# Optimization experiments

Hardware: AMD Instinct MI355X
Metric: run time of the kernel (lower is better)

The kernel has to match this reference:

```python
import jax, jax.numpy as jnp
import numpy as np

N, T, IN = 20000, 30, 32
H = 64          # lstm hidden
HEADS = 4
OUT = 32
E = 320000
NEG_SLOPE = 0.2


def _lstm_layer(x, Wih, Whh, bih, bhh):
    # x: [N, T, in]; Wih: [in, 4H]; Whh: [H, 4H]
    n, t, _ = x.shape
    h_dim = Whh.shape[0]
    xW = x @ Wih + bih  # [N, T, 4H]
    xW = jnp.transpose(xW, (1, 0, 2))  # [T, N, 4H]

    def step(carry, xt):
        h, c = carry
        g = xt + h @ Whh + bhh
        i, f, gg, o = jnp.split(g, 4, axis=-1)  # torch gate order i,f,g,o
        i = jax.nn.sigmoid(i)
        f = jax.nn.sigmoid(f)
        gg = jnp.tanh(gg)
        o = jax.nn.sigmoid(o)
        c = f * c + i * gg
        h = o * jnp.tanh(c)
        return (h, c), h

    init = (jnp.zeros((n, h_dim), x.dtype), jnp.zeros((n, h_dim), x.dtype))
    _, hs = jax.lax.scan(step, init, xW)
    return jnp.transpose(hs, (1, 0, 2))  # [N, T, H]


def _gat(x, edge_index, W, att_src, att_dst, bias, n):
    # x: [N, F_in]; W: [F_in, heads*C]; att_*: [heads, C]
    heads, C = att_src.shape
    h = (x @ W).reshape(n, heads, C)
    src, dst = edge_index[0], edge_index[1]
    a_src = jnp.einsum('nhc,hc->nh', h, att_src)  # [N, heads]
    a_dst = jnp.einsum('nhc,hc->nh', h, att_dst)
    logits = jax.nn.leaky_relu(a_src[src] + a_dst[dst], NEG_SLOPE)  # [E, heads]
    # segment softmax over destination nodes (every node has a self loop)
    m = jax.ops.segment_max(logits, dst, num_segments=n)
    e = jnp.exp(logits - m[dst])
    s = jax.ops.segment_sum(e, dst, num_segments=n)
    alpha = e / s[dst]
    out = jax.ops.segment_sum(alpha[:, :, None] * h[src], dst, num_segments=n)
    return out.reshape(n, heads * C) + bias


def setup_inputs() -> dict:
    key = jax.random.key(0)
    ks = jax.random.split(key, 20)
    sc = 0.05
    inp = {
        'x': jax.random.normal(ks[0], (N, T, IN), jnp.float32),
        'edge_index': jax.random.randint(ks[1], (2, E), 0, N, jnp.int64),
        # LSTM layer 0
        'Wih0': jax.random.normal(ks[2], (IN, 4 * H), jnp.float32) * sc,
        'Whh0': jax.random.normal(ks[3], (H, 4 * H), jnp.float32) * sc,
        'bih0': jnp.zeros((4 * H,), jnp.float32),
        'bhh0': jnp.zeros((4 * H,), jnp.float32),
        # LSTM layer 1
        'Wih1': jax.random.normal(ks[4], (H, 4 * H), jnp.float32) * sc,
        'Whh1': jax.random.normal(ks[5], (H, 4 * H), jnp.float32) * sc,
        'bih1': jnp.zeros((4 * H,), jnp.float32),
        'bhh1': jnp.zeros((4 * H,), jnp.float32),
        # GAT layer 1: H -> H per head, HEADS heads, concat
        'W1': jax.random.normal(ks[6], (H, HEADS * H), jnp.float32) * sc,
        'as1': jax.random.normal(ks[7], (HEADS, H), jnp.float32) * sc,
        'ad1': jax.random.normal(ks[8], (HEADS, H), jnp.float32) * sc,
        'b1': jnp.zeros((HEADS * H,), jnp.float32),
        # GAT layer 2: HEADS*H -> OUT, 1 head
        'W2': jax.random.normal(ks[9], (HEADS * H, OUT), jnp.float32) * sc,
        'as2': jax.random.normal(ks[10], (1, OUT), jnp.float32) * sc,
        'ad2': jax.random.normal(ks[11], (1, OUT), jnp.float32) * sc,
        'b2': jnp.zeros((OUT,), jnp.float32),
    }
    return inp


def reference(x, edge_index, Wih0, Whh0, bih0, bhh0, Wih1, Whh1, bih1, bhh1,
              W1, as1, ad1, b1, W2, as2, ad2, b2):
    n = x.shape[0]
    # add self loops (PyG GATConv default add_self_loops=True)
    loops = jnp.arange(n, dtype=edge_index.dtype)
    ei = jnp.concatenate([edge_index, jnp.stack([loops, loops])], axis=1)
    # 2-layer LSTM, take last timestep hidden state per node
    h = _lstm_layer(x, Wih0, Whh0, bih0, bhh0)
    h = _lstm_layer(h, Wih1, Whh1, bih1, bhh1)
    h = h[:, -1, :]  # [N, H]
    h = _gat(h, ei, W1, as1, ad1, b1, n)
    h = jax.nn.relu(h)
    out = _gat(h, ei, W2, as2, ad2, b2, n)
    return out
```

## Files before the change

### kernel.cpp

```cpp
#include <hip/hip_runtime.h>
#include <math.h>

#define Tt  30
#define INP 32
#define HID 64
#define NEG 0.2f
#define P   72

typedef __attribute__((ext_vector_type(8))) _Float16 half8;
typedef __attribute__((ext_vector_type(4))) float    f4;

#define MFMA16(a,b,c) __builtin_amdgcn_mfma_f32_16x16x32_f16((a),(b),(c),0,0,0)

__device__ __forceinline__ float fsigm(float v){ return __builtin_amdgcn_rcpf(1.f + __expf(-v)); }
__device__ __forceinline__ float ftanh(float v){ return 2.f * __builtin_amdgcn_rcpf(1.f + __expf(-2.f*v)) - 1.f; }

__device__ __forceinline__ float f16lo(unsigned u){
    union{unsigned short s; _Float16 f;} c; c.s = (unsigned short)(u & 0xffffu); return (float)c.f;
}
__device__ __forceinline__ float f16hi(unsigned u){
    union{unsigned short s; _Float16 f;} c; c.s = (unsigned short)(u >> 16); return (float)c.f;
}

__device__ __forceinline__ void loadW(const float* __restrict__ Wa, const float* __restrict__ Wb,
                                      int R0, int kt, int quad, int col, half8& H){
    #pragma unroll
    for (int e = 0; e < 8; ++e){
        int r = kt*32 + quad*8 + e;
        float v = (r < R0) ? Wa[r*256 + col] : Wb[(r - R0)*256 + col];
        H[e] = (_Float16)v;
    }
}

__global__ __launch_bounds__(256, 2) void k_lstm_fused(
    const float* __restrict__ x,
    const float* __restrict__ Wih0, const float* __restrict__ Whh0,
    const float* __restrict__ bih0, const float* __restrict__ bhh0,
    const float* __restrict__ Wih1, const float* __restrict__ Whh1,
    const float* __restrict__ bih1, const float* __restrict__ bhh1,
    float* __restrict__ h1last)
{
    __shared__ _Float16 sH0[2][16 * P];
    __shared__ _Float16 sH1[2][16 * P];

    const int tid = threadIdx.x, lane = tid & 63, j = tid >> 6;
    const int quad = lane >> 4, ln = lane & 15;
    const int jc = j * 16 + ln;
    const int n0 = blockIdx.x * 16;

    half8 w0[3][4];
    #pragma unroll
    for (int kt = 0; kt < 3; ++kt)
        #pragma unroll
        for (int g = 0; g < 4; ++g)
            loadW(Wih0, Whh0, 32, kt, quad, g*64 + jc, w0[kt][g]);

    half8 w1[4][4];
    #pragma unroll
    for (int kt = 0; kt < 4; ++kt)
        #pragma unroll
        for (int g = 0; g < 4; ++g)
            loadW(Wih1, Whh1, 64, kt, quad, g*64 + jc, w1[kt][g]);

    float b0[4], b1v[4];
    #pragma unroll
    for (int g = 0; g < 4; ++g){
        b0[g]  = bih0[g*64 + jc] + bhh0[g*64 + jc];
        b1v[g] = bih1[g*64 + jc] + bhh1[g*64 + jc];
    }

    float c0[4] = {0.f,0.f,0.f,0.f};
    float c1[4] = {0.f,0.f,0.f,0.f};

    for (int idx = tid; idx < 16*P; idx += 256){
        sH0[0][idx] = (_Float16)0.f; sH1[0][idx] = (_Float16)0.f;
    }
    __syncthreads();

    const float* xrow = x + (size_t)(n0 + ln) * (Tt*INP) + quad*8;
    float4 nxa = *(const float4*)xrow, nxb = *(const float4*)(xrow + 4);

    #pragma unroll 1
    for (int t = 0; t < Tt; ++t){
        const int pb = t & 1;
        _Float16* h0r = sH0[pb];
        _Float16* h0w = sH0[pb ^ 1];
        _Float16* h1r = sH1[pb];
        _Float16* h1w = sH1[pb ^ 1];

        float4 xa = nxa, xb = nxb;
        if (t + 1 < Tt){
            nxa = *(const float4*)(xrow + (t+1)*INP);
            nxb = *(const float4*)(xrow + (t+1)*INP + 4);
        }
        half8 xf;
        xf[0]=(_Float16)xa.x; xf[1]=(_Float16)xa.y; xf[2]=(_Float16)xa.z; xf[3]=(_Float16)xa.w;
        xf[4]=(_Float16)xb.x; xf[5]=(_Float16)xb.y; xf[6]=(_Float16)xb.z; xf[7]=(_Float16)xb.w;

        half8 h0a = *(const half8*)(h0r + ln*P + quad*8);
        half8 h0b = *(const half8*)(h0r + ln*P + 32 + quad*8);
        {
            f4 acc[4];
            #pragma unroll
            for (int g = 0; g < 4; ++g){
                f4 a = {b0[g], b0[g], b0[g], b0[g]};
                a = MFMA16(xf,  w0[0][g], a);
                a = MFMA16(h0a, w0[1][g], a);
                a = MFMA16(h0b, w0[2][g], a);
                acc[g] = a;
            }
            #pragma unroll
            for (int r = 0; r < 4; ++r){
                float iv = fsigm(acc[0][r]), fv = fsigm(acc[1][r]);
                float gv = ftanh(acc[2][r]), ov = fsigm(acc[3][r]);
                c0[r] = fv * c0[r] + iv * gv;
                h0w[(quad*4 + r)*P + jc] = (_Float16)(ov * ftanh(c0[r]));
            }
        }
        __syncthreads();

        half8 a0 = *(const half8*)(h0w + ln*P + quad*8);
        half8 a1 = *(const half8*)(h0w + ln*P + 32 + quad*8);
        half8 a2 = *(const half8*)(h1r + ln*P + quad*8);
        half8 a3 = *(const half8*)(h1r + ln*P + 32 + quad*8);
        {
            f4 acc[4];
            #pragma unroll
            for (int g = 0; g < 4; ++g){
                f4 a = {b1v[g], b1v[g], b1v[g], b1v[g]};
                a = MFMA16(a0, w1[0][g], a);
                a = MFMA16(a1, w1[1][g], a);
                a = MFMA16(a2, w1[2][g], a);
                a = MFMA16(a3, w1[3][g], a);
                acc[g] = a;
            }
            #pragma unroll
            for (int r = 0; r < 4; ++r){
                float iv = fsigm(acc[0][r]), fv = fsigm(acc[1][r]);
                float gv = ftanh(acc[2][r]), ov = fsigm(acc[3][r]);
                c1[r] = fv * c1[r] + iv * gv;
                float hv = ov * ftanh(c1[r]);
                h1w[(quad*4 + r)*P + jc] = (_Float16)hv;
                if (t == Tt-1) h1last[(size_t)(n0 + quad*4 + r)*HID + jc] = hv;
            }
        }
    }
}

__global__ __launch_bounds__(256) void k_gproj1(
    const float* __restrict__ hl, const float* __restrict__ W1,
    const float* __restrict__ as1, const float* __restrict__ ad1,
    _Float16* __restrict__ H1, float* __restrict__ a_s, float* __restrict__ a_d)
{
    __shared__ float sh[16][64];
    const int tid = threadIdx.x;
    const int n0 = blockIdx.x * 16;
    for (int idx = tid; idx < 16*64; idx += 256)
        sh[idx >> 6][idx & 63] = hl[(size_t)(n0 + (idx >> 6)) * 64 + (idx & 63)];
    __syncthreads();
    float acc[16];
    #pragma unroll
    for (int r = 0; r < 16; ++r) acc[r] = 0.f;
    for (int j = 0; j < 64; ++j){
        float w = W1[j * 256 + tid];
        #pragma unroll
        for (int r = 0; r < 16; ++r) acc[r] += sh[r][j] * w;
    }
    const float asv = as1[tid], adv = ad1[tid];
    const int wv = tid >> 6;
    #pragma unroll
    for (int r = 0; r < 16; ++r){
        H1[(size_t)(n0 + r) * 256 + tid] = (_Float16)acc[r];
        float ls = acc[r] * asv, ld = acc[r] * adv;
        #pragma unroll
        for (int off = 32; off >= 1; off >>= 1){ ls += __shfl_down(ls, off); ld += __shfl_down(ld, off); }
        if ((tid & 63) == 0){ a_s[(n0 + r) * 4 + wv] = ls; a_d[(n0 + r) * 4 + wv] = ld; }
    }
}

__global__ __launch_bounds__(256) void k_gproj2(
    const _Float16* __restrict__ h2, const float* __restrict__ W2,
    const float* __restrict__ as2, const float* __restrict__ ad2,
    _Float16* __restrict__ H2, float* __restrict__ a2s, float* __restrict__ a2d)
{
    __shared__ float sh[16][260];
    const int tid = threadIdx.x;
    const int n0 = blockIdx.x * 16;
    for (int idx = tid; idx < 16*256; idx += 256)
        sh[idx >> 8][idx & 255] = (float)h2[(size_t)(n0 + (idx >> 8)) * 256 + (idx & 255)];
    __syncthreads();
    const int c = tid & 31, rg = tid >> 5;
    float a0 = 0.f, a1 = 0.f;
    for (int j = 0; j < 256; ++j){
        float w = W2[j * 32 + c];
        a0 += sh[rg*2][j] * w;
        a1 += sh[rg*2 + 1][j] * w;
    }
    const float asv = as2[c], adv = ad2[c];
    H2[(size_t)(n0 + rg*2) * 32 + c]     = (_Float16)a0;
    H2[(size_t)(n0 + rg*2 + 1) * 32 + c] = (_Float16)a1;
    float s0 = a0 * asv, d0 = a0 * adv, s1 = a1 * asv, d1 = a1 * adv;
    #pragma unroll
    for (int off = 16; off >= 1; off >>= 1){
        s0 += __shfl_down(s0, off, 32); d0 += __shfl_down(d0, off, 32);
        s1 += __shfl_down(s1, off, 32); d1 += __shfl_down(d1, off, 32);
    }
    if (c == 0){
        a2s[n0 + rg*2] = s0;     a2d[n0 + rg*2] = d0;
        a2s[n0 + rg*2 + 1] = s1; a2d[n0 + rg*2 + 1] = d1;
    }
}

__global__ void k_count(const int* __restrict__ ei, int* __restrict__ deg, int E, int Et)
{
    int e = blockIdx.x * blockDim.x + threadIdx.x;
    if (e >= Et) return;
    int d = (e < E) ? ei[E + e] : e - E;
    atomicAdd(&deg[d], 1);
}

__global__ __launch_bounds__(256) void k_scanA(const int* __restrict__ deg, int* __restrict__ off,
                                               int* __restrict__ csum, int N)
{
    __shared__ int sm[256];
    int b = blockIdx.x, tid = threadIdx.x, i = b * 256 + tid;
    int v = (i < N) ? deg[i] : 0;
    sm[tid] = v;
    __syncthreads();
    #pragma unroll
    for (int s = 1; s < 256; s <<= 1) {
        int t = (tid >= s) ? sm[tid - s] : 0;
        __syncthreads();
        sm[tid] += t;
        __syncthreads();
    }
    if (i < N) off[i] = sm[tid] - v;
    if (tid == 255) csum[b] = sm[255];
}

__global__ __launch_bounds__(256) void k_scanB(int* __restrict__ csum, int NC)
{
    __shared__ int sm[256];
    const int tid = threadIdx.x;
    if (NC > 256){
        if (tid == 0){ int run = 0; for (int b = 0; b < NC; ++b){ int t = csum[b]; csum[b] = run; run += t; } }
        return;
    }
    int v = (tid < NC) ? csum[tid] : 0;
    sm[tid] = v;
    __syncthreads();
    #pragma unroll
    for (int s = 1; s < 256; s <<= 1){
        int t = (tid >= s) ? sm[tid - s] : 0;
        __syncthreads();
        sm[tid] += t;
        __syncthreads();
    }
    if (tid < NC) csum[tid] = sm[tid] - v;
}

__global__ __launch_bounds__(256) void k_scanC(int* __restrict__ off, const int* __restrict__ csum,
                                               int* __restrict__ cursor, int N)
{
    int i = blockIdx.x * blockDim.x + threadIdx.x;
    if (i < N){ int v = off[i] + csum[i >> 8]; off[i] = v; cursor[i] = v; }
}

__global__ void k_fill(const int* __restrict__ ei, int* __restrict__ cursor,
                       int* __restrict__ elist, int E, int Et)
{
    int e = blockIdx.x * blockDim.x + threadIdx.x;
    if (e >= Et) return;
    int s, d;
    if (e < E) { s = ei[e]; d = ei[E + e]; } else { s = d = e - E; }
    int slot = atomicAdd(&cursor[d], 1);
    elist[slot] = s;
}

__global__ __launch_bounds__(256) void k_gat1(
    const int* __restrict__ off, const int* __restrict__ deg, const int* __restrict__ elist,
    const float* __restrict__ a_s, const float* __restrict__ a_d,
    const _Float16* __restrict__ H1, const float* __restrict__ b1,
    _Float16* __restrict__ h2)
{
    __shared__ int   sSrc[256];
    __shared__ float sAl[256 * 4];
    __shared__ float sRed[256 * 3];
    const int d = blockIdx.x, tid = threadIdx.x;
    const int cp = tid & 127;
    const int ep = tid >> 7;
    const int hh = cp >> 5;
    const int base = off[d], n_e = deg[d];
    const unsigned* H1u = (const unsigned*)H1;

    float acc0 = 0.f, acc1 = 0.f, asum = 0.f;
    for (int c0 = 0; c0 < n_e; c0 += 256) {
        int nc = min(256, n_e - c0);
        if (tid < nc) sSrc[tid] = elist[base + c0 + tid];
        __syncthreads();
        for (int idx = tid; idx < nc * 4; idx += 256) {
            int e = idx >> 2, g = idx & 3;
            int s = sSrc[e];
            float a = a_s[s * 4 + g] + a_d[d * 4 + g];
            float l = a > 0.f ? a : NEG * a;
            sAl[idx] = __expf(l);
        }
        __syncthreads();
        int e = ep;
        for (; e + 2 < nc; e += 4) {
            int s0 = sSrc[e], s1 = sSrc[e + 2];
            float al0 = sAl[e * 4 + hh], al1 = sAl[(e + 2) * 4 + hh];
            unsigned u0 = H1u[(size_t)s0 * 128 + cp];
            unsigned u1 = H1u[(size_t)s1 * 128 + cp];
            acc0 += al0 * f16lo(u0); acc1 += al0 * f16hi(u0); asum += al0;
            acc0 += al1 * f16lo(u1); acc1 += al1 * f16hi(u1); asum += al1;
        }
        if (e < nc) {
            int s0 = sSrc[e];
            float al0 = sAl[e * 4 + hh];
            unsigned u0 = H1u[(size_t)s0 * 128 + cp];
            acc0 += al0 * f16lo(u0); acc1 += al0 * f16hi(u0); asum += al0;
        }
        __syncthreads();
    }
    sRed[tid] = acc0; sRed[256 + tid] = acc1; sRed[512 + tid] = asum;
    __syncthreads();
    if (ep == 0) {
        float A0 = acc0 + sRed[tid + 128];
        float A1 = acc1 + sRed[256 + tid + 128];
        float S  = asum + sRed[512 + tid + 128];
        float r = __builtin_amdgcn_rcpf(S);
        int c = cp * 2;
        float v0 = A0 * r + b1[c];
        float v1 = A1 * r + b1[c + 1];
        v0 = v0 > 0.f ? v0 : 0.f;
        v1 = v1 > 0.f ? v1 : 0.f;
        union { unsigned u; _Float16 f[2]; } pk;
        pk.f[0] = (_Float16)v0; pk.f[1] = (_Float16)v1;
        ((unsigned*)h2)[(size_t)d * 128 + cp] = pk.u;
    }
}

__global__ __launch_bounds__(256) void k_gat2(
    const int* __restrict__ off, const int* __restrict__ deg, const int* __restrict__ elist,
    const float* __restrict__ a2s, const float* __restrict__ a2d,
    const _Float16* __restrict__ H2, const float* __restrict__ b2,
    float* __restrict__ outp)
{
    const int d = blockIdx.x * 4 + (threadIdx.x >> 6);
    const int lane = threadIdx.x & 63;
    const int base = off[d], n_e = deg[d];
    const float add = a2d[d];
    const int half = lane >> 5, c = lane & 31;

    float acc = 0.f, asum = 0.f;
    int e = half;
    for (; e + 2 < n_e; e += 4) {
        int s0 = elist[base + e], s1 = elist[base + e + 2];
        float a0 = a2s[s0] + add, a1 = a2s[s1] + add;
        float l0 = a0 > 0.f ? a0 : NEG * a0, l1 = a1 > 0.f ? a1 : NEG * a1;
        float al0 = __expf(l0), al1 = __expf(l1);
        acc  += al0 * (float)H2[(size_t)s0 * 32 + c];
        acc  += al1 * (float)H2[(size_t)s1 * 32 + c];
        asum += al0 + al1;
    }
    if (e < n_e) {
        int s0 = elist[base + e];
        float a0 = a2s[s0] + add;
        float l0 = a0 > 0.f ? a0 : NEG * a0;
        float al0 = __expf(l0);
        acc  += al0 * (float)H2[(size_t)s0 * 32 + c];
        asum += al0;
    }
    acc  += __shfl_down(acc, 32);
    asum += __shfl_down(asum, 32);
    if (lane < 32) outp[(size_t)d * 32 + c] = acc * __builtin_amdgcn_rcpf(asum) + b2[c];
}

static inline int cdiv(long long a, long long b) { return (int)((a + b - 1) / b); }

extern "C" void kernel_launch(void* const* d_in, const int* in_sizes, int n_in,
                              void* d_out, int out_size, void* d_ws, size_t ws_size,
                              hipStream_t stream)
{
    const float* x    = (const float*)d_in[0];
    const int*   ei   = (const int*)d_in[1];
    const float* Wih0 = (const float*)d_in[2];
    const float* Whh0 = (const float*)d_in[3];
    const float* bih0 = (const float*)d_in[4];
    const float* bhh0 = (const float*)d_in[5];
    const float* Wih1 = (const float*)d_in[6];
    const float* Whh1 = (const float*)d_in[7];
    const float* bih1 = (const float*)d_in[8];
    const float* bhh1 = (const float*)d_in[9];
    const float* W1   = (const float*)d_in[10];
    const float* as1  = (const float*)d_in[11];
    const float* ad1  = (const float*)d_in[12];
    const float* b1   = (const float*)d_in[13];
    const float* W2   = (const float*)d_in[14];
    const float* as2  = (const float*)d_in[15];
    const float* ad2  = (const float*)d_in[16];
    const float* b2   = (const float*)d_in[17];
    float* outp = (float*)d_out;

    const int N  = in_sizes[0] / (Tt * INP);
    const int E  = in_sizes[1] / 2;
    const int Et = E + N;
    const int NC = cdiv(N, 256);

    float* ws = (float*)d_ws;
    float* h1last = ws;
    _Float16* H1 = (_Float16*)(h1last + (size_t)N * 64);
    _Float16* h2 = (_Float16*)((float*)H1 + (size_t)N * 256);
    _Float16* H2 = (_Float16*)((float*)h2 + (size_t)N * 256);
    float* as1p = (float*)H2 + (size_t)N * 32;
    float* ad1p = as1p + (size_t)N * 4;
    float* a2s  = ad1p + (size_t)N * 4;
    float* a2d  = a2s + N;
    int* deg    = (int*)(a2d + N);
    int* off    = deg + N;
    int* cursor = off + N;
    int* csum   = cursor + N;
    int* elist  = csum + NC;

    k_lstm_fused<<<dim3(N / 16), dim3(256), 0, stream>>>(
        x, Wih0, Whh0, bih0, bhh0, Wih1, Whh1, bih1, bhh1, h1last);

    hipMemsetAsync(deg, 0, (size_t)N * 4, stream);
    k_count<<<cdiv(Et, 256), 256, 0, stream>>>(ei, deg, E, Et);
    k_scanA<<<NC, 256, 0, stream>>>(deg, off, csum, N);
    k_scanB<<<1, 256, 0, stream>>>(csum, NC);
    k_scanC<<<NC, 256, 0, stream>>>(off, csum, cursor, N);
    k_fill<<<cdiv(Et, 256), 256, 0, stream>>>(ei, cursor, elist, E, Et);

    k_gproj1<<<dim3(N / 16), dim3(256), 0, stream>>>(h1last, W1, as1, ad1, H1, as1p, ad1p);
    k_gat1<<<dim3(N), dim3(256), 0, stream>>>(off, deg, elist, as1p, ad1p, H1, b1, h2);

    k_gproj2<<<dim3(N / 16), dim3(256), 0, stream>>>(h2, W2, as2, ad2, H2, a2s, a2d);
    k_gat2<<<dim3(N / 4), dim3(256), 0, stream>>>(off, deg, elist, a2s, a2d, H2, b2, outp);
}
```

Before: 383.9 us.

## Rewrite GAT layer-1 aggregation as one wavefront per destination node

The first GAT aggregation kernel changes from one 256-thread block per destination node, with shared-memory staging, barriers and a cross-half reduction, to one 64-lane wavefront per node and four nodes per block. Each lane now gathers four fp16 channels with a uint2 load and computes the attention exponentials inline, processing four edges per iteration. This removes the __syncthreads, LDS traffic and the mostly idle threads that came from an average degree of about 17 edges per node. In exchange, every lane recomputes the exp per edge for its head, and the a_s lookups are redundant across the lanes of a head.

```diff
diff --git a/kernel.cpp b/kernel.cpp
--- a/kernel.cpp
+++ b/kernel.cpp
@@ -281,64 +281,54 @@
     const int* __restrict__ off, const int* __restrict__ deg, const int* __restrict__ elist,
     const float* __restrict__ a_s, const float* __restrict__ a_d,
     const _Float16* __restrict__ H1, const float* __restrict__ b1,
-    _Float16* __restrict__ h2)
-{
-    __shared__ int   sSrc[256];
-    __shared__ float sAl[256 * 4];
-    __shared__ float sRed[256 * 3];
-    const int d = blockIdx.x, tid = threadIdx.x;
-    const int cp = tid & 127;
-    const int ep = tid >> 7;
-    const int hh = cp >> 5;
+    _Float16* __restrict__ h2, int N)
+{
+    const int d = blockIdx.x * 4 + (threadIdx.x >> 6);
+    if (d >= N) return;
+    const int lane = threadIdx.x & 63;
+    const int h = lane >> 4;
     const int base = off[d], n_e = deg[d];
-    const unsigned* H1u = (const unsigned*)H1;
-
-    float acc0 = 0.f, acc1 = 0.f, asum = 0.f;
-    for (int c0 = 0; c0 < n_e; c0 += 256) {
-        int nc = min(256, n_e - c0);
-        if (tid < nc) sSrc[tid] = elist[base + c0 + tid];
-        __syncthreads();
-        for (int idx = tid; idx < nc * 4; idx += 256) {
-            int e = idx >> 2, g = idx & 3;
-            int s = sSrc[e];
-            float a = a_s[s * 4 + g] + a_d[d * 4 + g];
-            float l = a > 0.f ? a : NEG * a;
-            sAl[idx] = __expf(l);
-        }
-        __syncthreads();
-        int e = ep;
-        for (; e + 2 < nc; e += 4) {
-            int s0 = sSrc[e], s1 = sSrc[e + 2];
-            float al0 = sAl[e * 4 + hh], al1 = sAl[(e + 2) * 4 + hh];
-            unsigned u0 = H1u[(size_t)s0 * 128 + cp];
-            unsigned u1 = H1u[(size_t)s1 * 128 + cp];
-            acc0 += al0 * f16lo(u0); acc1 += al0 * f16hi(u0); asum += al0;
-            acc0 += al1 * f16lo(u1); acc1 += al1 * f16hi(u1); asum += al1;
-        }
-        if (e < nc) {
-            int s0 = sSrc[e];
-            float al0 = sAl[e * 4 + hh];
-            unsigned u0 = H1u[(size_t)s0 * 128 + cp];
-            acc0 += al0 * f16lo(u0); acc1 += al0 * f16hi(u0); asum += al0;
-        }
-        __syncthreads();
-    }
-    sRed[tid] = acc0; sRed[256 + tid] = acc1; sRed[512 + tid] = asum;
-    __syncthreads();
-    if (ep == 0) {
-        float A0 = acc0 + sRed[tid + 128];
-        float A1 = acc1 + sRed[256 + tid + 128];
-        float S  = asum + sRed[512 + tid + 128];
-        float r = __builtin_amdgcn_rcpf(S);
-        int c = cp * 2;
-        float v0 = A0 * r + b1[c];
-        float v1 = A1 * r + b1[c + 1];
-        v0 = v0 > 0.f ? v0 : 0.f;
-        v1 = v1 > 0.f ? v1 : 0.f;
-        union { unsigned u; _Float16 f[2]; } pk;
-        pk.f[0] = (_Float16)v0; pk.f[1] = (_Float16)v1;
-        ((unsigned*)h2)[(size_t)d * 128 + cp] = pk.u;
-    }
+    const float add = a_d[d * 4 + h];
+    const uint2* H1v = (const uint2*)H1;
+
+    float acc0 = 0.f, acc1 = 0.f, acc2 = 0.f, acc3 = 0.f, asum = 0.f;
+    int e = 0;
+    for (; e + 4 <= n_e; e += 4) {
+        int s0 = elist[base + e],     s1 = elist[base + e + 1];
+        int s2 = elist[base + e + 2], s3 = elist[base + e + 3];
+        float A0 = a_s[s0 * 4 + h] + add, A1 = a_s[s1 * 4 + h] + add;
+        float A2 = a_s[s2 * 4 + h] + add, A3 = a_s[s3 * 4 + h] + add;
+        uint2 u0 = H1v[(size_t)s0 * 64 + lane], u1 = H1v[(size_t)s1 * 64 + lane];
+        uint2 u2 = H1v[(size_t)s2 * 64 + lane], u3 = H1v[(size_t)s3 * 64 + lane];
+        float l0 = A0 > 0.f ? A0 : NEG * A0, l1 = A1 > 0.f ? A1 : NEG * A1;
+        float l2 = A2 > 0.f ? A2 : NEG * A2, l3 = A3 > 0.f ? A3 : NEG * A3;
+        float al0 = __expf(l0), al1 = __expf(l1), al2 = __expf(l2), al3 = __expf(l3);
+        acc0 += al0*f16lo(u0.x) + al1*f16lo(u1.x) + al2*f16lo(u2.x) + al3*f16lo(u3.x);
+        acc1 += al0*f16hi(u0.x) + al1*f16hi(u1.x) + al2*f16hi(u2.x) + al3*f16hi(u3.x);
+        acc2 += al0*f16lo(u0.y) + al1*f16lo(u1.y) + al2*f16lo(u2.y) + al3*f16lo(u3.y);
+        acc3 += al0*f16hi(u0.y) + al1*f16hi(u1.y) + al2*f16hi(u2.y) + al3*f16hi(u3.y);
+        asum += al0 + al1 + al2 + al3;
+    }
+    for (; e < n_e; ++e) {
+        int s0 = elist[base + e];
+        float A0 = a_s[s0 * 4 + h] + add;
+        uint2 u0 = H1v[(size_t)s0 * 64 + lane];
+        float l0 = A0 > 0.f ? A0 : NEG * A0;
+        float al0 = __expf(l0);
+        acc0 += al0 * f16lo(u0.x); acc1 += al0 * f16hi(u0.x);
+        acc2 += al0 * f16lo(u0.y); acc3 += al0 * f16hi(u0.y);
+        asum += al0;
+    }
+    const float r = __builtin_amdgcn_rcpf(asum);
+    const float4 bv = *(const float4*)(b1 + lane * 4);
+    float v0 = acc0 * r + bv.x, v1 = acc1 * r + bv.y;
+    float v2 = acc2 * r + bv.z, v3 = acc3 * r + bv.w;
+    v0 = v0 > 0.f ? v0 : 0.f; v1 = v1 > 0.f ? v1 : 0.f;
+    v2 = v2 > 0.f ? v2 : 0.f; v3 = v3 > 0.f ? v3 : 0.f;
+    union { uint2 u; _Float16 f[4]; } pk;
+    pk.f[0] = (_Float16)v0; pk.f[1] = (_Float16)v1;
+    pk.f[2] = (_Float16)v2; pk.f[3] = (_Float16)v3;
+    ((uint2*)h2)[(size_t)d * 64 + lane] = pk.u;
 }
 
 __global__ __launch_bounds__(256) void k_gat2(
@@ -434,7 +424,7 @@
     k_fill<<<cdiv(Et, 256), 256, 0, stream>>>(ei, cursor, elist, E, Et);
 
     k_gproj1<<<dim3(N / 16), dim3(256), 0, stream>>>(h1last, W1, as1, ad1, H1, as1p, ad1p);
-    k_gat1<<<dim3(N), dim3(256), 0, stream>>>(off, deg, elist, as1p, ad1p, H1, b1, h2);
+    k_gat1<<<dim3(cdiv(N, 4)), dim3(256), 0, stream>>>(off, deg, elist, as1p, ad1p, H1, b1, h2, N);
 
     k_gproj2<<<dim3(N / 16), dim3(256), 0, stream>>>(h2, W2, as2, ad2, H2, a2s, a2d);
     k_gat2<<<dim3(N / 4), dim3(256), 0, stream>>>(off, deg, elist, a2s, a2d, H2, b2, outp);
```

Result: faster. 374.2 us (-2.5%).
